# Optimization experiments

Hardware: AMD Instinct MI355X
Metric: run time of the kernel (lower is better)

Reference implementation:

```python
import jax, jax.numpy as jnp
import numpy as np

D = 512      # d_model
H = 8        # num_heads
HD = D // H  # head_dim = 64 (concat makes per-head dim 2*HD=128)
B = 32       # batch*group
T = 512      # time steps


def setup_inputs() -> dict:
    key = jax.random.key(0)
    ks = jax.random.split(key, 18)
    def W(k):
        return jax.random.normal(k, (D, D), dtype=jnp.float32) * 0.02
    inp = {
        "x_face": jax.random.normal(ks[0], (B, T, D), dtype=jnp.float32),
        "x_skeleton": jax.random.normal(ks[1], (B, T, D), dtype=jnp.float32),
        "wq1": W(ks[2]), "bq1": jnp.zeros((D,), jnp.float32),
        "wk1": W(ks[3]), "bk1": jnp.zeros((D,), jnp.float32),
        "wv1": W(ks[4]), "bv1": jnp.zeros((D,), jnp.float32),
        "wq2": W(ks[5]), "bq2": jnp.zeros((D,), jnp.float32),
        "wk2": W(ks[6]), "bk2": jnp.zeros((D,), jnp.float32),
        "wv2": W(ks[7]), "bv2": jnp.zeros((D,), jnp.float32),
        "wo1": W(ks[8]), "bo1": jnp.zeros((D,), jnp.float32),
        "wo2": W(ks[9]), "bo2": jnp.zeros((D,), jnp.float32),
    }
    return inp


def reference(x_face, x_skeleton,
              wq1, bq1, wk1, bk1, wv1, bv1,
              wq2, bq2, wk2, bk2, wv2, bv2,
              wo1, bo1, wo2, bo2):
    Bt, Tt, _ = x_face.shape

    def proj(x, w, b):
        # torch Linear: x @ W^T + b, then 'b t (h d) -> b h t d'
        return (x @ w.T + b).reshape(Bt, Tt, H, HD).transpose(0, 2, 1, 3)

    q = jnp.concatenate([proj(x_face, wq1, bq1), proj(x_skeleton, wq2, bq2)], axis=3)  # [B,H,T,2*HD]
    k = jnp.concatenate([proj(x_face, wk1, bk1), proj(x_skeleton, wk2, bk2)], axis=3)
    v = jnp.concatenate([proj(x_face, wv1, bv1), proj(x_skeleton, wv2, bv2)], axis=3)

    scores = jnp.einsum('bhid,bhjd->bhij', q, k) / (HD ** 0.5)  # scale by head_dim**0.5 as in source
    attn = jax.nn.softmax(scores, axis=-1)                      # dropout = identity (eval mode)
    out = jnp.einsum('bhij,bhjd->bhid', attn, v)                # [B,H,T,2*HD]
    out = out.transpose(0, 2, 1, 3).reshape(Bt, Tt, 2 * D)      # 'b h t d -> b t (h d)'

    x1, x2 = out[..., :D], out[..., D:]
    return (x1 @ wo1.T + bo1, x2 @ wo2.T + bo2)
```

## Files before the change

kernel.cpp:

```cpp
#include <hip/hip_runtime.h>
#include <hip/hip_bf16.h>
#include <stdint.h>

typedef __hip_bfloat16 bf16;
using f32x4 = __attribute__((ext_vector_type(4))) float;
using s16x8 = __attribute__((ext_vector_type(8))) short;

typedef __attribute__((address_space(1))) unsigned int gu32;
typedef __attribute__((address_space(3))) unsigned int lu32;

__device__ __forceinline__ void gll16(const void* g, void* l) {
  __builtin_amdgcn_global_load_lds((const gu32*)g, (lu32*)l, 16, 0, 0);
}

struct ConvJob { const float* src; bf16* dst; int n4; int pad; };
struct ConvParams { ConvJob j[10]; };
struct alignas(8) Bf4 { bf16 v[4]; };

__global__ void convert_kernel(ConvParams p) {
  ConvJob jb = p.j[blockIdx.z];
  int stride = gridDim.x * blockDim.x;
  for (int i = blockIdx.x * blockDim.x + threadIdx.x; i < jb.n4; i += stride) {
    float4 v = ((const float4*)jb.src)[i];
    Bf4 o;
    o.v[0] = __float2bfloat16(v.x);
    o.v[1] = __float2bfloat16(v.y);
    o.v[2] = __float2bfloat16(v.z);
    o.v[3] = __float2bfloat16(v.w);
    ((Bf4*)jb.dst)[i] = o;
  }
}

struct GemmSlice {
  const bf16* A; const bf16* W; const float* bias;
  bf16* dstQ; float* dstF;
  long lda; int dhalf; float scale; int mode;
};
struct GemmParams { GemmSlice s[6]; };

#define STG_A(v, h) do { \
    const bf16* s_ = Ab + (v) * 64 + (h) * 32; \
    bf16* d_ = lds + (((v) & 1) << 14) + (h) * 8192 + tid * 8; \
    gll16(s_, d_); gll16(s_ + (lda << 7), d_ + 4096); \
  } while (0)

#define STG_B(v, h) do { \
    const bf16* s_ = Wb + (v) * 64 + (h) * 32; \
    bf16* d_ = lds + 32768 + (((v) & 1) << 14) + (h) * 8192 + tid * 8; \
    gll16(s_, d_); gll16(s_ + (512 << 7), d_ + 4096); \
  } while (0)

#define GP(MB, H, RDB, STAGE_STMT, WAIT_STMT) do { \
    if (RDB) { \
      _Pragma("unroll") \
      for (int nj_ = 0; nj_ < 4; ++nj_) \
        bfr[nj_] = *(const s16x8*)(bB + (H) * 8192 + brow32 + nj_ * 512 + cw); \
    } \
    s16x8 af[4]; \
    _Pragma("unroll") \
    for (int i_ = 0; i_ < 4; ++i_) \
      af[i_] = *(const s16x8*)(bA + (H) * 8192 + arow32 + ((MB) + i_) * 512 + cw); \
    STAGE_STMT; \
    __builtin_amdgcn_s_barrier(); \
    asm volatile("s_waitcnt lgkmcnt(0)" ::: "memory"); \
    __builtin_amdgcn_sched_barrier(0); \
    __builtin_amdgcn_s_setprio(1); \
    _Pragma("unroll") \
    for (int i_ = 0; i_ < 4; ++i_) \
      _Pragma("unroll") \
      for (int nj_ = 0; nj_ < 4; ++nj_) \
        acc[(MB) + i_][nj_] = __builtin_amdgcn_mfma_f32_16x16x32_bf16(af[i_], bfr[nj_], acc[(MB) + i_][nj_], 0, 0, 0); \
    __builtin_amdgcn_s_setprio(0); \
    WAIT_STMT; \
    __builtin_amdgcn_s_barrier(); \
  } while (0)

__global__ __launch_bounds__(512, 2) void gemm_kernel(GemmParams p) {
  __shared__ alignas(16) bf16 lds[65536];
  const GemmSlice sl = p.s[blockIdx.z];
  const long lda = sl.lda;
  const int tid = threadIdx.x;
  const int w = tid >> 6, ln = tid & 63;
  const int fr = ln & 15, fq = ln >> 4;
  const int wm = w >> 2, wn = w & 3;
  const int gm0 = blockIdx.x * 256;
  const int gn0 = blockIdx.y * 256;
  const int r0 = tid >> 2;
  const int c0 = ((tid & 3) ^ (r0 & 3)) * 8;
  const bf16* const Ab = sl.A + (long)(gm0 + r0) * lda + c0;
  const bf16* const Wb = sl.W + (long)(gn0 + r0) * 512 + c0;
  const int cw = (fq ^ (fr & 3)) * 8;
  const int arow32 = (wm * 128 + fr) * 32;
  const int brow32 = (wn * 64 + fr) * 32;

  f32x4 acc[8][4] = {};

  STG_B(0, 0); STG_A(0, 0); STG_B(0, 1); STG_A(0, 1);
  __builtin_amdgcn_sched_barrier(0);
  STG_B(1, 0); STG_A(1, 0); STG_B(1, 1);
  asm volatile("s_waitcnt vmcnt(8)" ::: "memory");
  __builtin_amdgcn_sched_barrier(0);
  __builtin_amdgcn_s_barrier();

#pragma unroll
  for (int u = 0; u < 8; ++u) {
    const bf16* bA = lds + ((u & 1) << 14);
    const bf16* bB = lds + 32768 + ((u & 1) << 14);
    s16x8 bfr[4];
    GP(0, 0, 1, { if (u <= 6) STG_A(u + 1, 1); }, {});
    GP(4, 0, 0, { if (u <= 5) STG_B(u + 2, 0); },
       { if (u <= 6) { asm volatile("s_waitcnt vmcnt(6)" ::: "memory"); }
         else        { asm volatile("s_waitcnt vmcnt(0)" ::: "memory"); }
         __builtin_amdgcn_sched_barrier(0); });
    GP(0, 1, 1, { if (u <= 5) STG_A(u + 2, 0); }, {});
    GP(4, 1, 0, { if (u <= 5) STG_B(u + 2, 1); },
       { if (u <= 5)      { asm volatile("s_waitcnt vmcnt(8)" ::: "memory"); __builtin_amdgcn_sched_barrier(0); }
         else if (u == 6) { asm volatile("s_waitcnt vmcnt(2)" ::: "memory"); __builtin_amdgcn_sched_barrier(0); } });
  }

  if (sl.mode == 0) {
#pragma unroll
    for (int mi = 0; mi < 8; ++mi)
#pragma unroll
      for (int nj = 0; nj < 4; ++nj) {
        const int col = gn0 + wn * 64 + nj * 16 + fr;
        const int h = col >> 6;
        const int dd = (col & 63) + sl.dhalf;
        const float bia = sl.bias[col];
#pragma unroll
        for (int r = 0; r < 4; ++r) {
          const int row = gm0 + wm * 128 + mi * 16 + fq * 4 + r;
          const int b = row >> 9, t = row & 511;
          const float v = (acc[mi][nj][r] + bia) * sl.scale;
          sl.dstQ[(((long)(b * 8 + h) * 512 + t) << 7) + dd] = __float2bfloat16(v);
        }
      }
  } else if (sl.mode == 2) {
#pragma unroll
    for (int mi = 0; mi < 8; ++mi)
#pragma unroll
      for (int nj = 0; nj < 4; ++nj) {
        const int col = gn0 + wn * 64 + nj * 16 + fr;
        const int h = col >> 6;
        const int dd = (col & 63) + sl.dhalf;
        const float bia = sl.bias[col];
        const int row0 = gm0 + wm * 128 + mi * 16 + fq * 4;
        const int b = row0 >> 9, t = row0 & 511;
        Bf4 o;
#pragma unroll
        for (int r = 0; r < 4; ++r) o.v[r] = __float2bfloat16(acc[mi][nj][r] + bia);
        *(Bf4*)(sl.dstQ + (((long)(b * 8 + h) * 128 + dd) << 9) + t) = o;
      }
  } else {
#pragma unroll
    for (int mi = 0; mi < 8; ++mi)
#pragma unroll
      for (int nj = 0; nj < 4; ++nj) {
        const int col = gn0 + wn * 64 + nj * 16 + fr;
        const float bia = sl.bias[col];
#pragma unroll
        for (int r = 0; r < 4; ++r) {
          const int row = gm0 + wm * 128 + mi * 16 + fq * 4 + r;
          sl.dstF[(long)row * 512 + col] = acc[mi][nj][r] + bia;
        }
      }
  }
}

#define STAGE(kt, bK, bV) do { \
    _Pragma("unroll") \
    for (int p_ = 0; p_ < 4; ++p_) \
      gll16(kgb + (kt) * 8192 + p_ * 2048, (bK) + tid * 8 + p_ * 2048); \
    _Pragma("unroll") \
    for (int p_ = 0; p_ < 4; ++p_) \
      gll16(vgb + (kt) * 64 + p_ * 16384, (bV) + tid * 8 + p_ * 2048); \
  } while (0)

#define COMPUTE(bK, bV) do { \
  f32x4 s2[2][4] = {}; \
  _Pragma("unroll") \
  for (int ks = 0; ks < 4; ++ks) { \
    _Pragma("unroll") \
    for (int ni = 0; ni < 4; ++ni) { \
      const int row_ = ni * 16 + fr; \
      const s16x8 kf = *(const s16x8*)((bK) + row_ * 128 + ((ks * 32 + fq * 8) ^ ((row_ & 7) << 3))); \
      _Pragma("unroll") \
      for (int mi = 0; mi < 2; ++mi) \
        s2[mi][ni] = __builtin_amdgcn_mfma_f32_16x16x32_bf16(qf[mi][ks], kf, s2[mi][ni], 0, 0, 0); \
    } \
  } \
  _Pragma("unroll") \
  for (int mi = 0; mi < 2; ++mi) \
    _Pragma("unroll") \
    for (int r = 0; r < 4; ++r) { \
      float ps = 0.f; \
      _Pragma("unroll") \
      for (int ni = 0; ni < 4; ++ni) { \
        const float pe = __builtin_amdgcn_exp2f(s2[mi][ni][r]); \
        s2[mi][ni][r] = pe; ps += pe; \
      } \
      ps += __shfl_xor(ps, 1); ps += __shfl_xor(ps, 2); \
      ps += __shfl_xor(ps, 4); ps += __shfl_xor(ps, 8); \
      lrow[mi][r] += ps; \
    } \
  _Pragma("unroll") \
  for (int mi = 0; mi < 2; ++mi) \
    _Pragma("unroll") \
    for (int ni = 0; ni < 4; ++ni) \
      _Pragma("unroll") \
      for (int r = 0; r < 4; ++r) { \
        const int rp = mi * 16 + fq * 4 + r; \
        sPw[rp * 64 + ((ni * 16 + fr) ^ ((rp & 7) << 3))] = __float2bfloat16(s2[mi][ni][r]); \
      } \
  _Pragma("unroll") \
  for (int ks = 0; ks < 2; ++ks) { \
    s16x8 pf[2]; \
    _Pragma("unroll") \
    for (int mi = 0; mi < 2; ++mi) { \
      const int row_ = mi * 16 + fr; \
      pf[mi] = *(const s16x8*)(sPw + row_ * 64 + ((ks * 32 + fq * 8) ^ ((row_ & 7) << 3))); \
    } \
    _Pragma("unroll") \
    for (int nj = 0; nj < 8; ++nj) { \
      const int row_ = nj * 16 + fr; \
      const s16x8 vf = *(const s16x8*)((bV) + row_ * 64 + ((ks * 32 + fq * 8) ^ ((row_ & 7) << 3))); \
      _Pragma("unroll") \
      for (int mi = 0; mi < 2; ++mi) \
        o[mi][nj] = __builtin_amdgcn_mfma_f32_16x16x32_bf16(pf[mi], vf, o[mi][nj], 0, 0, 0); \
    } \
  } \
} while (0)

__global__ __launch_bounds__(256, 2) void attn_kernel(const bf16* __restrict__ Q,
                                                      const bf16* __restrict__ K,
                                                      const bf16* __restrict__ Vt,
                                                      bf16* __restrict__ AO) {
  __shared__ alignas(16) bf16 lds[40960];
  bf16* const ldsK0 = lds;
  bf16* const ldsV0 = lds + 8192;
  bf16* const ldsK1 = lds + 16384;
  bf16* const ldsV1 = lds + 24576;
  bf16* const sP    = lds + 32768;
  const int tid = threadIdx.x;
  const int w = tid >> 6, ln = tid & 63;
  const int fr = ln & 15, fq = ln >> 4;
  const int lg = (blockIdx.x & 7) * 128 + (blockIdx.x >> 3);
  const int bh = lg >> 2;
  const int q0 = (lg & 3) * 128;
  const long base = (long)bh << 16;
  bf16* const sPw = sP + w * 2048;

  const int kr0 = tid >> 4, kc = tid & 15;
  const int vr0 = tid >> 3, vc = tid & 7;
  const bf16* const kgb = K + base + kr0 * 128 + ((kc ^ (kr0 & 7)) * 8);
  const bf16* const vgb = Vt + base + (long)vr0 * 512 + ((vc ^ (vr0 & 7)) * 8);

  {
    const bf16* const qgb = Q + base + (long)q0 * 128 + kr0 * 128 + ((kc ^ (kr0 & 7)) * 8);
#pragma unroll
    for (int p = 0; p < 8; ++p)
      gll16(qgb + p * 2048, lds + tid * 8 + p * 2048);
  }
  __syncthreads();
  s16x8 qf[2][4];
#pragma unroll
  for (int mi = 0; mi < 2; ++mi) {
    const int row = w * 32 + mi * 16 + fr;
#pragma unroll
    for (int ks = 0; ks < 4; ++ks)
      qf[mi][ks] = *(const s16x8*)(lds + row * 128 + ((ks * 32 + fq * 8) ^ ((row & 7) << 3)));
  }
  __syncthreads();

  f32x4 o[2][8] = {};
  float lrow[2][4] = {};

  STAGE(0, ldsK0, ldsV0);
  STAGE(1, ldsK1, ldsV1);

  for (int kt = 0; kt < 7; ++kt) {
    const bf16* bK = (kt & 1) ? ldsK1 : ldsK0;
    const bf16* bV = (kt & 1) ? ldsV1 : ldsV0;
    asm volatile("s_waitcnt vmcnt(8)" ::: "memory");
    __builtin_amdgcn_sched_barrier(0);
    __builtin_amdgcn_s_barrier();
    COMPUTE(bK, bV);
    asm volatile("s_waitcnt lgkmcnt(0)" ::: "memory");
    __builtin_amdgcn_sched_barrier(0);
    __builtin_amdgcn_s_barrier();
    if (kt < 6) STAGE(kt + 2, (bf16*)bK, (bf16*)bV);
  }
  asm volatile("s_waitcnt vmcnt(0)" ::: "memory");
  __builtin_amdgcn_sched_barrier(0);
  __builtin_amdgcn_s_barrier();
  COMPUTE(ldsK1, ldsV1);

  const int b = bh >> 3, h = bh & 7;
  float rl[2][4];
#pragma unroll
  for (int mi = 0; mi < 2; ++mi)
#pragma unroll
    for (int r = 0; r < 4; ++r) rl[mi][r] = 1.f / lrow[mi][r];
#pragma unroll
  for (int mi = 0; mi < 2; ++mi)
#pragma unroll
    for (int nj = 0; nj < 8; ++nj) {
      const int col = h * 128 + nj * 16 + fr;
#pragma unroll
      for (int r = 0; r < 4; ++r) {
        const int trow = q0 + w * 32 + mi * 16 + fq * 4 + r;
        AO[((long)(b * 512 + trow) << 10) + col] = __float2bfloat16(o[mi][nj][r] * rl[mi][r]);
      }
    }
}

extern "C" void kernel_launch(void* const* d_in, const int* in_sizes, int n_in,
                              void* d_out, int out_size, void* d_ws, size_t ws_size,
                              hipStream_t stream) {
  const float* xf = (const float*)d_in[0];
  const float* xs = (const float*)d_in[1];
  const float* w_f[8] = { (const float*)d_in[2], (const float*)d_in[4], (const float*)d_in[6],
                          (const float*)d_in[8], (const float*)d_in[10], (const float*)d_in[12],
                          (const float*)d_in[14], (const float*)d_in[16] };

  bf16* ws = (bf16*)d_ws;
  bf16* XF = ws;
  bf16* XS = ws + 8388608;
  bf16* WW = ws + 16777216;
  bf16* Qb = ws + 18874368;
  bf16* Kb = Qb + 16777216;
  bf16* Vb = Kb + 16777216;
  bf16* AO = ws;

  ConvParams cp;
  cp.j[0] = { xf, XF, 2097152, 0 };
  cp.j[1] = { xs, XS, 2097152, 0 };
  for (int i = 0; i < 8; ++i) cp.j[2 + i] = { w_f[i], WW + i * 262144, 65536, 0 };
  convert_kernel<<<dim3(512, 1, 10), 256, 0, stream>>>(cp);

  const float qsc = 0.125f * 1.44269504088896f;
  GemmParams gp;
  gp.s[0] = { XF, WW + 0 * 262144, (const float*)d_in[3],  Qb, nullptr, 512, 0,  qsc, 0 };
  gp.s[1] = { XS, WW + 3 * 262144, (const float*)d_in[9],  Qb, nullptr, 512, 64, qsc, 0 };
  gp.s[2] = { XF, WW + 1 * 262144, (const float*)d_in[5],  Kb, nullptr, 512, 0,  1.f, 0 };
  gp.s[3] = { XS, WW + 4 * 262144, (const float*)d_in[11], Kb, nullptr, 512, 64, 1.f, 0 };
  gp.s[4] = { XF, WW + 2 * 262144, (const float*)d_in[7],  Vb, nullptr, 512, 0,  1.f, 2 };
  gp.s[5] = { XS, WW + 5 * 262144, (const float*)d_in[13], Vb, nullptr, 512, 64, 1.f, 2 };
  gemm_kernel<<<dim3(64, 2, 6), 512, 0, stream>>>(gp);

  attn_kernel<<<dim3(1024), 256, 0, stream>>>(Qb, Kb, Vb, AO);

  float* out = (float*)d_out;
  GemmParams op;
  op.s[0] = { AO,       WW + 6 * 262144, (const float*)d_in[15], nullptr, out,           1024, 0, 1.f, 1 };
  op.s[1] = { AO + 512, WW + 7 * 262144, (const float*)d_in[17], nullptr, out + 8388608, 1024, 0, 1.f, 1 };
  op.s[2] = op.s[0]; op.s[3] = op.s[0]; op.s[4] = op.s[0]; op.s[5] = op.s[0];
  gemm_kernel<<<dim3(64, 2, 2), 512, 0, stream>>>(op);
}
```

Measured before the change: 179.1 us.

## Restructure GEMM LDS tiles to full-K64 rows with 8-way swizzle and reordered pipeline

Changes the LDS staging layout from two K-halves of 32 columns to row-major 64-wide K tiles split by M/N halves, with an 8-wide XOR swizzle. The main loop is reorganised into four quadrant MFMA phases that reuse A and B fragments across phases, with new prefetch ordering and vmcnt waits. The aim is to cut LDS reads and improve overlap of global-to-LDS loads with MFMA work. It adds extra barriers and changes the wait counts, which risks stalls or hazards if the counts are wrong.

```diff
diff --git a/kernel.cpp b/kernel.cpp
--- a/kernel.cpp
+++ b/kernel.cpp
@@ -38,42 +38,51 @@
 };
 struct GemmParams { GemmSlice s[6]; };
 
-#define STG_A(v, h) do { \
-    const bf16* s_ = Ab + (v) * 64 + (h) * 32; \
-    bf16* d_ = lds + (((v) & 1) << 14) + (h) * 8192 + tid * 8; \
-    gll16(s_, d_); gll16(s_ + (lda << 7), d_ + 4096); \
-  } while (0)
-
-#define STG_B(v, h) do { \
-    const bf16* s_ = Wb + (v) * 64 + (h) * 32; \
-    bf16* d_ = lds + 32768 + (((v) & 1) << 14) + (h) * 8192 + tid * 8; \
-    gll16(s_, d_); gll16(s_ + (512 << 7), d_ + 4096); \
-  } while (0)
-
-#define GP(MB, H, RDB, STAGE_STMT, WAIT_STMT) do { \
-    if (RDB) { \
-      _Pragma("unroll") \
-      for (int nj_ = 0; nj_ < 4; ++nj_) \
-        bfr[nj_] = *(const s16x8*)(bB + (H) * 8192 + brow32 + nj_ * 512 + cw); \
-    } \
-    s16x8 af[4]; \
+#define STG_A(kt, h) do { \
+    const bf16* s_ = Ab + (long)((h) * 128) * lda + (kt) * 64; \
+    bf16* d_ = lds + (((kt) & 1) << 14) + (h) * 8192 + tid * 8; \
+    gll16(s_, d_); gll16(s_ + (lda << 6), d_ + 4096); \
+  } while (0)
+
+#define STG_B(kt, h) do { \
+    const bf16* s_ = Wb + (long)((h) * 128) * 512 + (kt) * 64; \
+    bf16* d_ = lds + 32768 + (((kt) & 1) << 14) + (h) * 8192 + tid * 8; \
+    gll16(s_, d_); gll16(s_ + (512 << 6), d_ + 4096); \
+  } while (0)
+
+#define RD_A(MB) do { \
+    _Pragma("unroll") \
+    for (int i_ = 0; i_ < 4; ++i_) { \
+      const bf16* rp_ = bA + (wm * 128 + ((MB) + i_) * 16 + fr) * 64; \
+      aF[i_][0] = *(const s16x8*)(rp_ + cw0); \
+      aF[i_][1] = *(const s16x8*)(rp_ + cw1); \
+    } \
+  } while (0)
+
+#define RD_B(NB, DST) do { \
+    _Pragma("unroll") \
+    for (int j_ = 0; j_ < 2; ++j_) { \
+      const bf16* rp_ = bB + (wn * 64 + ((NB) + j_) * 16 + fr) * 64; \
+      DST[j_][0] = *(const s16x8*)(rp_ + cw0); \
+      DST[j_][1] = *(const s16x8*)(rp_ + cw1); \
+    } \
+  } while (0)
+
+#define MM(MB, NB, BF) do { \
+    __builtin_amdgcn_s_setprio(1); \
     _Pragma("unroll") \
     for (int i_ = 0; i_ < 4; ++i_) \
-      af[i_] = *(const s16x8*)(bA + (H) * 8192 + arow32 + ((MB) + i_) * 512 + cw); \
-    STAGE_STMT; \
-    __builtin_amdgcn_s_barrier(); \
-    asm volatile("s_waitcnt lgkmcnt(0)" ::: "memory"); \
-    __builtin_amdgcn_sched_barrier(0); \
-    __builtin_amdgcn_s_setprio(1); \
-    _Pragma("unroll") \
-    for (int i_ = 0; i_ < 4; ++i_) \
-      _Pragma("unroll") \
-      for (int nj_ = 0; nj_ < 4; ++nj_) \
-        acc[(MB) + i_][nj_] = __builtin_amdgcn_mfma_f32_16x16x32_bf16(af[i_], bfr[nj_], acc[(MB) + i_][nj_], 0, 0, 0); \
+      _Pragma("unroll") \
+      for (int j_ = 0; j_ < 2; ++j_) { \
+        acc[(MB) + i_][(NB) + j_] = __builtin_amdgcn_mfma_f32_16x16x32_bf16(aF[i_][0], BF[j_][0], acc[(MB) + i_][(NB) + j_], 0, 0, 0); \
+        acc[(MB) + i_][(NB) + j_] = __builtin_amdgcn_mfma_f32_16x16x32_bf16(aF[i_][1], BF[j_][1], acc[(MB) + i_][(NB) + j_], 0, 0, 0); \
+      } \
     __builtin_amdgcn_s_setprio(0); \
-    WAIT_STMT; \
-    __builtin_amdgcn_s_barrier(); \
-  } while (0)
+  } while (0)
+
+#define BAR __builtin_amdgcn_s_barrier()
+#define LGKM0 do { asm volatile("s_waitcnt lgkmcnt(0)" ::: "memory"); \
+                   __builtin_amdgcn_sched_barrier(0); } while (0)
 
 __global__ __launch_bounds__(512, 2) void gemm_kernel(GemmParams p) {
   __shared__ alignas(16) bf16 lds[65536];
@@ -85,37 +94,48 @@
   const int wm = w >> 2, wn = w & 3;
   const int gm0 = blockIdx.x * 256;
   const int gn0 = blockIdx.y * 256;
-  const int r0 = tid >> 2;
-  const int c0 = ((tid & 3) ^ (r0 & 3)) * 8;
+  const int r0 = tid >> 3;
+  const int c0 = ((tid & 7) ^ (r0 & 7)) * 8;
   const bf16* const Ab = sl.A + (long)(gm0 + r0) * lda + c0;
   const bf16* const Wb = sl.W + (long)(gn0 + r0) * 512 + c0;
-  const int cw = (fq ^ (fr & 3)) * 8;
-  const int arow32 = (wm * 128 + fr) * 32;
-  const int brow32 = (wn * 64 + fr) * 32;
+  const int cw0 = (fq * 8) ^ ((fr & 7) * 8);
+  const int cw1 = (32 + fq * 8) ^ ((fr & 7) * 8);
 
   f32x4 acc[8][4] = {};
 
-  STG_B(0, 0); STG_A(0, 0); STG_B(0, 1); STG_A(0, 1);
+  STG_A(0, 0); STG_A(0, 1); STG_B(0, 0); STG_B(0, 1);
   __builtin_amdgcn_sched_barrier(0);
-  STG_B(1, 0); STG_A(1, 0); STG_B(1, 1);
-  asm volatile("s_waitcnt vmcnt(8)" ::: "memory");
+  STG_B(1, 0); STG_B(1, 1);
+  asm volatile("s_waitcnt vmcnt(4)" ::: "memory");
   __builtin_amdgcn_sched_barrier(0);
-  __builtin_amdgcn_s_barrier();
+  BAR;
 
 #pragma unroll
   for (int u = 0; u < 8; ++u) {
     const bf16* bA = lds + ((u & 1) << 14);
     const bf16* bB = lds + 32768 + ((u & 1) << 14);
-    s16x8 bfr[4];
-    GP(0, 0, 1, { if (u <= 6) STG_A(u + 1, 1); }, {});
-    GP(4, 0, 0, { if (u <= 5) STG_B(u + 2, 0); },
-       { if (u <= 6) { asm volatile("s_waitcnt vmcnt(6)" ::: "memory"); }
-         else        { asm volatile("s_waitcnt vmcnt(0)" ::: "memory"); }
-         __builtin_amdgcn_sched_barrier(0); });
-    GP(0, 1, 1, { if (u <= 5) STG_A(u + 2, 0); }, {});
-    GP(4, 1, 0, { if (u <= 5) STG_B(u + 2, 1); },
-       { if (u <= 5)      { asm volatile("s_waitcnt vmcnt(8)" ::: "memory"); __builtin_amdgcn_sched_barrier(0); }
-         else if (u == 6) { asm volatile("s_waitcnt vmcnt(2)" ::: "memory"); __builtin_amdgcn_sched_barrier(0); } });
+    s16x8 aF[4][2], b01[2][2], b23[2][2];
+    RD_A(0); RD_B(0, b01);
+    if (u < 7) STG_A(u + 1, 0);
+    BAR; LGKM0;
+    MM(0, 0, b01);
+    BAR;
+    RD_B(2, b23);
+    if (u < 7) STG_A(u + 1, 1);
+    BAR; LGKM0;
+    MM(0, 2, b23);
+    BAR;
+    RD_A(4);
+    if (u < 6) STG_B(u + 2, 0);
+    BAR; LGKM0;
+    MM(4, 0, b01);
+    BAR;
+    if (u < 6) STG_B(u + 2, 1);
+    BAR; LGKM0;
+    MM(4, 2, b23);
+    if (u < 6)       { asm volatile("s_waitcnt vmcnt(4)" ::: "memory"); __builtin_amdgcn_sched_barrier(0); }
+    else if (u == 6) { asm volatile("s_waitcnt vmcnt(0)" ::: "memory"); __builtin_amdgcn_sched_barrier(0); }
+    BAR;
   }
 
   if (sl.mode == 0) {
```

Result: faster. 171.7 us (-4.1%).
